# Kernel tuning notes

Hardware: AMD Instinct MI355X
Metric: run time of the kernel (lower is better)

## Reference

```python
import jax, jax.numpy as jnp
import numpy as np

BS, SEQ, IN, H = 16, 1024, 512, 512


def setup_inputs() -> dict:
    key = jax.random.key(0)
    ks = jax.random.split(key, 10)
    std = 1.0 / np.sqrt(H)
    u = lambda k, shape: jax.random.uniform(k, shape, jnp.float32, -std, std)
    return {
        "x": jax.random.normal(ks[0], (BS, SEQ, IN), jnp.float32),
        # input projection fc: input_size -> hidden_size
        "Wfc": u(ks[1], (IN, H)),
        "bfc": u(ks[2], (H,)),
        # cell 1 (main hidden stream h): tree of matmuls + gated elementwise
        "W1x": u(ks[3], (2 * H, H)),  # layer-0 cells see duplicated features (2H)
        "W1h": u(ks[4], (H, H)),
        "W1g": u(ks[5], (H, H)),
        # cell 2 (second hidden stream c)
        "W2x": u(ks[6], (2 * H, H)),
        "W2h": u(ks[7], (H, H)),
        "W2g": u(ks[8], (H, H)),
    }


def reference(x, Wfc, bfc, W1x, W1h, W1g, W2x, W2h, W2g):
    bs = x.shape[0]
    # layer-0 input prep: fc projection then feature duplication (cat([x,x],dim=2))
    xp = x @ Wfc + bfc                      # [bs, seq, H]
    xp = jnp.concatenate([xp, xp], axis=-1)  # [bs, seq, 2H]
    xs = jnp.swapaxes(xp, 0, 1)             # [seq, bs, 2H] for scan over time

    h0 = jnp.zeros((bs, H), x.dtype)
    c0 = jnp.zeros((bs, H), x.dtype)

    def step(carry, x_t):
        h, c = carry  # hidden streams x2, x3 fed to each evolved cell
        h_new = jnp.tanh(x_t @ W1x + h @ W1h + jax.nn.sigmoid(c @ W1g) * h)
        c_new = jax.nn.sigmoid(x_t @ W2x + c @ W2h) * jnp.tanh(h @ W2g)
        return (h_new, c_new), h_new  # hidden_seq collects stream 0

    (h_fin, c_fin), hseq = jax.lax.scan(step, (h0, c0), xs)
    out = jnp.swapaxes(hseq, 0, 1)  # batch_first: [bs, seq, H]
    # final hidden states: [num_layers*(1), bs, H] per main stream
    return out, h_fin[None], c_fin[None]
```

## Files before the change

kernel.cpp:

```cpp
#include <hip/hip_runtime.h>


typedef unsigned short u16;
typedef unsigned int   u32;
typedef __attribute__((ext_vector_type(8))) short s8v;
typedef __attribute__((ext_vector_type(4))) float f4v;

__device__ __forceinline__ u16 f2bf_rne(float f){
  u32 u = __float_as_uint(f);
  u32 r = u + 0x7fffu + ((u >> 16) & 1u);
  return (u16)(r >> 16);
}
__device__ __forceinline__ float bf2f(u16 h){ return __uint_as_float(((u32)h) << 16); }
__device__ __forceinline__ f4v MFMA(s8v a, s8v b, f4v c){
  return __builtin_amdgcn_mfma_f32_16x16x32_bf16(a, b, c, 0, 0, 0);
}
__device__ __forceinline__ float sigmoidf_(float x){ return 1.0f / (1.0f + __expf(-x)); }
__device__ __forceinline__ float tanh_fast(float x){
  float e = __expf(2.0f * x);
  return 1.0f - 2.0f / (e + 1.0f);
}

template<bool CC> __device__ __forceinline__ s8v ld16(const u16* p){
  s8v r;
  if (CC) asm volatile("global_load_dwordx4 %0, %1, off sc0 sc1" : "=v"(r) : "v"(p));
  else    asm volatile("global_load_dwordx4 %0, %1, off"         : "=v"(r) : "v"(p));
  return r;
}
template<bool CC> __device__ __forceinline__ void st2(u16* p, u32 v){
  if (CC) asm volatile("global_store_short %0, %1, off sc0 sc1" :: "v"(p), "v"(v) : "memory");
  else    asm volatile("global_store_short %0, %1, off"         :: "v"(p), "v"(v) : "memory");
}
__device__ __forceinline__ void store_dword_cc(u32* p, u32 v){
  asm volatile("global_store_dword %0, %1, off sc0 sc1" :: "v"(p), "v"(v) : "memory");
}
__device__ __forceinline__ void store_dword_plain_wait(u32* p, u32 v){
  asm volatile("global_store_dword %0, %1, off\n\ts_waitcnt vmcnt(0)"
               :: "v"(p), "v"(v) : "memory");
}
__device__ __forceinline__ u32 load_dword_plain_wait(const u32* p){
  u32 r;
  asm volatile("global_load_dword %0, %1, off\n\ts_waitcnt vmcnt(0)"
               : "=v"(r) : "v"(p));
  return r;
}

#define SEQT 1024
#define NWG  16
#define PROT 16

static const size_t OFF_U1  = 0;
static const size_t OFF_U2  = 33554432;
static const size_t OFF_WCT = OFF_U2 + 16777216;
static const size_t OFF_ST  = OFF_WCT;
static const size_t OFF_WT  = OFF_WCT + 1048576;
static const size_t OFF_BC  = OFF_WT + 2097152;
static const size_t OFF_FL  = OFF_BC + 4096;
static const size_t OFF_TOK = OFF_FL + 65536;
static const size_t OFF_PRS = OFF_TOK + 4096;
static const size_t OFF_CTL = OFF_PRS + 4096;
static const size_t OFF_CN  = OFF_CTL + 4096;
static const size_t OFF_HCN = OFF_CN + 4096;
static const size_t OFF_CCN = OFF_HCN + 131072;

__global__ void wcombk(const float* __restrict__ Wfc, const float* __restrict__ W1x,
                       const float* __restrict__ W2x, u16* __restrict__ Wct){
  __shared__ float A[16][17], B[16][17];
  const float* Wx = blockIdx.z ? W2x : W1x;
  int i0 = blockIdx.y * 16, n0 = blockIdx.x * 16;
  int tx = threadIdx.x, ty = threadIdx.y;
  float acc = 0.f;
  for (int kc = 0; kc < 512; kc += 16){
    A[ty][tx] = Wfc[(size_t)(i0 + ty) * 512 + kc + tx];
    B[ty][tx] = Wx[(size_t)(kc + ty) * 512 + n0 + tx]
              + Wx[(size_t)(kc + ty + 512) * 512 + n0 + tx];
    __syncthreads();
    #pragma unroll
    for (int kk = 0; kk < 16; ++kk) acc += A[ty][kk] * B[kk][tx];
    __syncthreads();
  }
  Wct[(size_t)(blockIdx.z * 512 + n0 + tx) * 512 + i0 + ty] = f2bf_rne(acc);
}

__global__ void bcombk(const float* __restrict__ bfc, const float* __restrict__ W1x,
                       const float* __restrict__ W2x, float* __restrict__ bc){
  int n = blockIdx.x * 256 + threadIdx.x;
  const float* Wx = (n < 512) ? W1x : W2x;
  int nl = n & 511;
  float acc = 0.f;
  for (int k = 0; k < 512; ++k)
    acc += bfc[k] * (Wx[(size_t)k * 512 + nl] + Wx[(size_t)(k + 512) * 512 + nl]);
  bc[n] = acc;
}

__global__ void wtk(const float* __restrict__ A, const float* __restrict__ B,
                    const float* __restrict__ C, const float* __restrict__ D,
                    u16* __restrict__ Wt){
  __shared__ float tile[32][33];
  const float* src = (blockIdx.z == 0) ? A : (blockIdx.z == 1) ? B
                    : (blockIdx.z == 2) ? C : D;
  int n0 = blockIdx.x * 32, k0 = blockIdx.y * 32;
  for (int i = threadIdx.y; i < 32; i += 8)
    tile[i][threadIdx.x] = src[(size_t)(k0 + i) * 512 + n0 + threadIdx.x];
  __syncthreads();
  for (int i = threadIdx.y; i < 32; i += 8)
    Wt[(size_t)blockIdx.z * 262144 + (size_t)(n0 + i) * 512 + k0 + threadIdx.x]
        = f2bf_rne(tile[threadIdx.x][i]);
}

__global__ __launch_bounds__(256) void gemmk(
    const float* __restrict__ x, const u16* __restrict__ Wct,
    const float* __restrict__ bc, float* __restrict__ U1, u16* __restrict__ U2){
  int l = threadIdx.x & 63, w = threadIdx.x >> 6;
  int lr = l & 15, lk = l >> 4;
  int m0 = blockIdx.y * 128 + (w & 1) * 64;
  int n0 = blockIdx.x * 64 + (w >> 1) * 32;
  f4v acc[4][2] = {};
  for (int ks = 0; ks < 16; ++ks){
    int k0 = ks * 32 + lk * 8;
    s8v bh0 = *(const s8v*)(Wct + (size_t)(n0 + lr) * 512 + k0);
    s8v bh1 = *(const s8v*)(Wct + (size_t)(n0 + 16 + lr) * 512 + k0);
    #pragma unroll
    for (int mi = 0; mi < 4; ++mi){
      const float* xp = x + (size_t)(m0 + mi * 16 + lr) * 512 + k0;
      f4v v0 = *(const f4v*)xp;
      f4v v1 = *(const f4v*)(xp + 4);
      s8v ah, al;
      #pragma unroll
      for (int j = 0; j < 4; ++j){
        { u32 u = __float_as_uint(v0[j]); ah[j] = (short)(u >> 16);
          float lof = v0[j] - __uint_as_float(u & 0xffff0000u);
          al[j] = (short)(__float_as_uint(lof) >> 16); }
        { u32 u = __float_as_uint(v1[j]); ah[j + 4] = (short)(u >> 16);
          float lof = v1[j] - __uint_as_float(u & 0xffff0000u);
          al[j + 4] = (short)(__float_as_uint(lof) >> 16); }
      }
      acc[mi][0] = MFMA(ah, bh0, acc[mi][0]);
      acc[mi][0] = MFMA(al, bh0, acc[mi][0]);
      acc[mi][1] = MFMA(ah, bh1, acc[mi][1]);
      acc[mi][1] = MFMA(al, bh1, acc[mi][1]);
    }
  }
  #pragma unroll
  for (int mi = 0; mi < 4; ++mi)
    #pragma unroll
    for (int ni = 0; ni < 2; ++ni){
      int n = n0 + ni * 16 + lr;
      float badd = bc[n];
      #pragma unroll
      for (int j = 0; j < 4; ++j){
        int r = m0 + mi * 16 + lk * 4 + j;
        int b = r >> 10, t = r & 1023;
        size_t oi = (size_t)(t * 16 + b) * 512;
        float v = acc[mi][ni][j] + badd;
        if (n < 512) U1[oi + n] = v;
        else         U2[oi + n - 512] = f2bf_rne(v);
      }
    }
}

__device__ __forceinline__ void poll_cnt(u32* p, u32 need, int l){
  int g = 0;
  for (;;){
    u32 v = 0;
    if (l == 0)
      v = __hip_atomic_fetch_add(p, 0x10000u, __ATOMIC_RELAXED,
                                 __HIP_MEMORY_SCOPE_WORKGROUP);
    v = __builtin_amdgcn_readfirstlane(v);
    if ((v & 0xffffu) >= need) break;
    if (++g > 4000000) break;
    __builtin_amdgcn_s_sleep(1);
  }
}
__device__ __forceinline__ void tok_store(u32* tok, u32 v){
  __hip_atomic_store(tok, v, __ATOMIC_RELEASE, __HIP_MEMORY_SCOPE_WORKGROUP);
}
__device__ __forceinline__ void spin_tok(u32* tok, u32 need){
  int g = 0;
  while (__hip_atomic_load(tok, __ATOMIC_ACQUIRE, __HIP_MEMORY_SCOPE_WORKGROUP) < need){
    if (++g > 16000000) break;
  }
}

__device__ __forceinline__ void heater(const u32* done){
  float a0 = 1.0f + (float)(threadIdx.x & 7) * 1e-7f;
  float a1 = 1.5f;
  float m = 0.9999999f, b = 1e-7f;
  for (int it = 0; it < 600000; ++it){
    #pragma unroll
    for (int k = 0; k < 32; ++k){
      asm volatile("v_fmac_f32 %0, %2, %3\n\tv_fmac_f32 %1, %2, %3"
                   : "+v"(a0), "+v"(a1) : "v"(m), "v"(b));
    }
    if ((it & 15) == 0){
      if (__hip_atomic_load(done, __ATOMIC_RELAXED, __HIP_MEMORY_SCOPE_AGENT) != 0u)
        break;
    }
  }
  asm volatile("" :: "v"(a0), "v"(a1));
}

__device__ __forceinline__ void scan_fast(
    int wg, int tid,
    const float* __restrict__ U1, const u16* __restrict__ U2,
    const u16* __restrict__ Wt, u16* __restrict__ st,
    u32* __restrict__ hcnt, u32* __restrict__ ccnt,
    float* __restrict__ out, float* xg, float* xt, u32* ltok){
  const int w = tid >> 6, l = tid & 63;
  const int lr = l & 15, lk = l >> 4;
  const int ncol0 = wg * 32 + lr;

  s8v bf0[16], bf1[16];
  {
    const u16* Wm = Wt + (size_t)w * (512 * 512);
    #pragma unroll
    for (int ks = 0; ks < 16; ++ks){
      bf0[ks] = *(const s8v*)(Wm + (size_t)ncol0 * 512 + ks * 32 + lk * 8);
      bf1[ks] = *(const s8v*)(Wm + (size_t)(ncol0 + 16) * 512 + ks * 32 + lk * 8);
    }
  }
  const bool useH = (w == 0) || (w == 3);
  float hp0[4] = {0, 0, 0, 0}, hp1[4] = {0, 0, 0, 0};

  float un0[4], un1[4], uc0[4], uc1[4];
  u32   ur0[4], ur1[4];
  if (w == 0){
    #pragma unroll
    for (int j = 0; j < 4; ++j){
      size_t ro = (size_t)(lk * 4 + j) * 512;
      un0[j] = U1[ro + ncol0];
      un1[j] = U1[ro + ncol0 + 16];
    }
  } else if (w == 2){
    #pragma unroll
    for (int j = 0; j < 4; ++j){
      size_t ro = (size_t)(lk * 4 + j) * 512;
      ur0[j] = U2[ro + ncol0];
      ur1[j] = U2[ro + ncol0 + 16];
    }
  }

  for (int t = 0; t < SEQT; ++t){
    if (w == 0){
      if (t > 0) poll_cnt(hcnt + (size_t)(t - 1) * 32, NWG, l);
      tok_store(ltok + 0, (u32)(t + 1));
    } else if (w == 2){
      if (t > 0) poll_cnt(ccnt + (size_t)(t - 1) * 32, NWG, l);
      tok_store(ltok + 1, (u32)(t + 1));
    } else if (w == 3){
      spin_tok(ltok + 0, (u32)(t + 1));
    } else {
      spin_tok(ltok + 1, (u32)(t + 1));
    }
    __builtin_amdgcn_sched_barrier(0);

    u16* rb = st + (size_t)(t & (PROT - 1)) * 32768 + (useH ? 0 : 16384);
    s8v ah[16], al[16];
    {
      u16* bhp = rb + lr * 512 + lk * 8;
      u16* blp = rb + 8192 + lr * 512 + lk * 8;
      #pragma unroll
      for (int ks = 0; ks < 16; ++ks){
        ah[ks] = ld16<false>(bhp + ks * 32);
        al[ks] = ld16<false>(blp + ks * 32);
      }
    }
    asm volatile("s_waitcnt vmcnt(0)" ::: "memory");
    __builtin_amdgcn_sched_barrier(0);

    if (w == 0){
      #pragma unroll
      for (int j = 0; j < 4; ++j){ uc0[j] = un0[j]; uc1[j] = un1[j]; }
    } else if (w == 2){
      #pragma unroll
      for (int j = 0; j < 4; ++j){
        uc0[j] = __uint_as_float(ur0[j] << 16);
        uc1[j] = __uint_as_float(ur1[j] << 16);
      }
    }

    f4v a0 = {0, 0, 0, 0}, a1 = {0, 0, 0, 0};
    f4v b0 = {0, 0, 0, 0}, b1 = {0, 0, 0, 0};
    #pragma unroll
    for (int ks = 0; ks < 16; ++ks){
      a0 = MFMA(ah[ks], bf0[ks], a0);
      a1 = MFMA(ah[ks], bf1[ks], a1);
      b0 = MFMA(al[ks], bf0[ks], b0);
      b1 = MFMA(al[ks], bf1[ks], b1);
    }
    #pragma unroll
    for (int j = 0; j < 4; ++j){ a0[j] += b0[j]; a1[j] += b1[j]; }

    const int par = t & 1;
    u16* wb = st + (size_t)((t + 1) & (PROT - 1)) * 32768;
    const int tn = (t + 1 < SEQT) ? t + 1 : t;

    if (w == 1){
      #pragma unroll
      for (int j = 0; j < 4; ++j){
        xg[((par * 2 + 0) * 16 + lk * 4 + j) * 16 + lr] = sigmoidf_(a0[j]);
        xg[((par * 2 + 1) * 16 + lk * 4 + j) * 16 + lr] = sigmoidf_(a1[j]);
      }
      tok_store(ltok + 2, (u32)(t + 1));
    } else if (w == 3){
      #pragma unroll
      for (int j = 0; j < 4; ++j){
        xt[((par * 2 + 0) * 16 + lk * 4 + j) * 16 + lr] = tanh_fast(a0[j]);
        xt[((par * 2 + 1) * 16 + lk * 4 + j) * 16 + lr] = tanh_fast(a1[j]);
      }
      tok_store(ltok + 3, (u32)(t + 1));
    } else if (w == 0){
      spin_tok(ltok + 2, (u32)(t + 1));
      __builtin_amdgcn_sched_barrier(0);
      float hn0v[4], hn1v[4];
      #pragma unroll
      for (int j = 0; j < 4; ++j){
        int b = lk * 4 + j;
        float hn0 = tanh_fast(uc0[j] + a0[j] + xg[((par * 2 + 0) * 16 + b) * 16 + lr] * hp0[j]);
        float hn1 = tanh_fast(uc1[j] + a1[j] + xg[((par * 2 + 1) * 16 + b) * 16 + lr] * hp1[j]);
        hp0[j] = hn0; hp1[j] = hn1;
        hn0v[j] = hn0; hn1v[j] = hn1;
        u32 u0 = __float_as_uint(hn0), u1 = __float_as_uint(hn1);
        int bi = b * 512;
        st2<false>(wb + bi + ncol0,      u0 >> 16);
        st2<false>(wb + bi + ncol0 + 16, u1 >> 16);
        float lo0 = hn0 - __uint_as_float(u0 & 0xffff0000u);
        float lo1 = hn1 - __uint_as_float(u1 & 0xffff0000u);
        st2<false>(wb + 8192 + bi + ncol0,      __float_as_uint(lo0) >> 16);
        st2<false>(wb + 8192 + bi + ncol0 + 16, __float_as_uint(lo1) >> 16);
      }
      #pragma unroll
      for (int j = 0; j < 4; ++j){
        size_t ro = (size_t)(tn * 16 + lk * 4 + j) * 512;
        un0[j] = U1[ro + ncol0];
        un1[j] = U1[ro + ncol0 + 16];
      }
      asm volatile("s_waitcnt vmcnt(8)" ::: "memory");
      if (l == 0)
        __hip_atomic_fetch_add(hcnt + (size_t)t * 32, 1u,
                               __ATOMIC_RELAXED, __HIP_MEMORY_SCOPE_WORKGROUP);
      #pragma unroll
      for (int j = 0; j < 4; ++j){
        int b = lk * 4 + j;
        size_t ob = (size_t)b * (SEQT * 512) + (size_t)t * 512;
        out[ob + ncol0]      = hn0v[j];
        out[ob + ncol0 + 16] = hn1v[j];
        if (t == SEQT - 1){
          out[8388608 + (size_t)b * 512 + ncol0]      = hn0v[j];
          out[8388608 + (size_t)b * 512 + ncol0 + 16] = hn1v[j];
        }
      }
    } else {
      spin_tok(ltok + 3, (u32)(t + 1));
      __builtin_amdgcn_sched_barrier(0);
      float cn0v[4], cn1v[4];
      #pragma unroll
      for (int j = 0; j < 4; ++j){
        int b = lk * 4 + j;
        float cn0 = sigmoidf_(uc0[j] + a0[j]) * xt[((par * 2 + 0) * 16 + b) * 16 + lr];
        float cn1 = sigmoidf_(uc1[j] + a1[j]) * xt[((par * 2 + 1) * 16 + b) * 16 + lr];
        cn0v[j] = cn0; cn1v[j] = cn1;
        u32 u0 = __float_as_uint(cn0), u1 = __float_as_uint(cn1);
        int bi = b * 512;
        st2<false>(wb + 16384 + bi + ncol0,      u0 >> 16);
        st2<false>(wb + 16384 + bi + ncol0 + 16, u1 >> 16);
        float lo0 = cn0 - __uint_as_float(u0 & 0xffff0000u);
        float lo1 = cn1 - __uint_as_float(u1 & 0xffff0000u);
        st2<false>(wb + 24576 + bi + ncol0,      __float_as_uint(lo0) >> 16);
        st2<false>(wb + 24576 + bi + ncol0 + 16, __float_as_uint(lo1) >> 16);
      }
      #pragma unroll
      for (int j = 0; j < 4; ++j){
        size_t ro = (size_t)(tn * 16 + lk * 4 + j) * 512;
        ur0[j] = U2[ro + ncol0];
        ur1[j] = U2[ro + ncol0 + 16];
      }
      asm volatile("s_waitcnt vmcnt(8)" ::: "memory");
      if (l == 0)
        __hip_atomic_fetch_add(ccnt + (size_t)t * 32, 1u,
                               __ATOMIC_RELAXED, __HIP_MEMORY_SCOPE_WORKGROUP);
      if (t == SEQT - 1){
        #pragma unroll
        for (int j = 0; j < 4; ++j){
          int b = lk * 4 + j;
          out[8396800 + (size_t)b * 512 + ncol0]      = cn0v[j];
          out[8396800 + (size_t)b * 512 + ncol0 + 16] = cn1v[j];
        }
      }
    }
  }
}

__device__ __forceinline__ void scan_cc(
    int wg, int tid,
    const float* __restrict__ U1, const u16* __restrict__ U2,
    const u16* __restrict__ Wt, u16* __restrict__ st,
    u32* __restrict__ flags, float* __restrict__ out, float* xg, float* xt){
  const int w = tid >> 6, l = tid & 63;
  const int lr = l & 15, lk = l >> 4;
  const int ncol0 = wg * 32 + lr;
  s8v bf0[16], bf1[16];
  {
    const u16* Wm = Wt + (size_t)w * (512 * 512);
    #pragma unroll
    for (int ks = 0; ks < 16; ++ks){
      bf0[ks] = *(const s8v*)(Wm + (size_t)ncol0 * 512 + ks * 32 + lk * 8);
      bf1[ks] = *(const s8v*)(Wm + (size_t)(ncol0 + 16) * 512 + ks * 32 + lk * 8);
    }
  }
  const bool useH = (w == 0) || (w == 3);
  float hp0[4] = {0, 0, 0, 0}, hp1[4] = {0, 0, 0, 0};
  long guard = 0;
  for (int t = 0; t < SEQT; ++t){
    float uu0[4], uu1[4];
    if (w == 0){
      #pragma unroll
      for (int j = 0; j < 4; ++j){
        size_t ro = (size_t)(t * 16 + lk * 4 + j) * 512;
        uu0[j] = U1[ro + ncol0];
        uu1[j] = U1[ro + ncol0 + 16];
      }
    } else if (w == 2){
      #pragma unroll
      for (int j = 0; j < 4; ++j){
        size_t ro = (size_t)(t * 16 + lk * 4 + j) * 512;
        uu0[j] = bf2f(U2[ro + ncol0]);
        uu1[j] = bf2f(U2[ro + ncol0 + 16]);
      }
    }
    if (t > 0){
      const u32* fl = flags + (size_t)(t - 1) * NWG;
      for (;;){
        u32 v = 1u;
        if (l < NWG) v = __hip_atomic_load(fl + l, __ATOMIC_RELAXED, __HIP_MEMORY_SCOPE_AGENT);
        if (__all(v != 0u)) break;
        if (++guard > 1000000L) break;
      }
      __builtin_amdgcn_sched_barrier(0);
    }
    u16* rb = st + (size_t)(t & (PROT - 1)) * 32768 + (useH ? 0 : 16384);
    s8v ah[16], al[16];
    {
      u16* bhp = rb + lr * 512 + lk * 8;
      u16* blp = rb + 8192 + lr * 512 + lk * 8;
      #pragma unroll
      for (int ks = 0; ks < 16; ++ks){
        ah[ks] = ld16<true>(bhp + ks * 32);
        al[ks] = ld16<true>(blp + ks * 32);
      }
    }
    asm volatile("s_waitcnt vmcnt(0)" ::: "memory");
    __builtin_amdgcn_sched_barrier(0);
    f4v a0 = {0, 0, 0, 0}, a1 = {0, 0, 0, 0};
    f4v b0 = {0, 0, 0, 0}, b1 = {0, 0, 0, 0};
    #pragma unroll
    for (int ks = 0; ks < 16; ++ks){
      a0 = MFMA(ah[ks], bf0[ks], a0);
      a1 = MFMA(ah[ks], bf1[ks], a1);
      b0 = MFMA(al[ks], bf0[ks], b0);
      b1 = MFMA(al[ks], bf1[ks], b1);
    }
    #pragma unroll
    for (int j = 0; j < 4; ++j){ a0[j] += b0[j]; a1[j] += b1[j]; }
    if (w == 1){
      #pragma unroll
      for (int j = 0; j < 4; ++j){
        xg[(0 * 16 + lk * 4 + j) * 16 + lr] = sigmoidf_(a0[j]);
        xg[(1 * 16 + lk * 4 + j) * 16 + lr] = sigmoidf_(a1[j]);
      }
    } else if (w == 3){
      #pragma unroll
      for (int j = 0; j < 4; ++j){
        xt[(0 * 16 + lk * 4 + j) * 16 + lr] = tanh_fast(a0[j]);
        xt[(1 * 16 + lk * 4 + j) * 16 + lr] = tanh_fast(a1[j]);
      }
    }
    __syncthreads();
    u16* wb = st + (size_t)((t + 1) & (PROT - 1)) * 32768;
    float hn0v[4], hn1v[4], cn0v[4], cn1v[4];
    if (w == 0){
      #pragma unroll
      for (int j = 0; j < 4; ++j){
        int b = lk * 4 + j;
        float hn0 = tanh_fast(uu0[j] + a0[j] + xg[(0 * 16 + b) * 16 + lr] * hp0[j]);
        float hn1 = tanh_fast(uu1[j] + a1[j] + xg[(1 * 16 + b) * 16 + lr] * hp1[j]);
        hp0[j] = hn0; hp1[j] = hn1;
        hn0v[j] = hn0; hn1v[j] = hn1;
        u32 u0 = __float_as_uint(hn0), u1 = __float_as_uint(hn1);
        int bi = b * 512;
        st2<true>(wb + bi + ncol0,      u0 >> 16);
        st2<true>(wb + bi + ncol0 + 16, u1 >> 16);
        float lo0 = hn0 - __uint_as_float(u0 & 0xffff0000u);
        float lo1 = hn1 - __uint_as_float(u1 & 0xffff0000u);
        st2<true>(wb + 8192 + bi + ncol0,      __float_as_uint(lo0) >> 16);
        st2<true>(wb + 8192 + bi + ncol0 + 16, __float_as_uint(lo1) >> 16);
      }
      asm volatile("s_waitcnt vmcnt(0)" ::: "memory");
    } else if (w == 2){
      #pragma unroll
      for (int j = 0; j < 4; ++j){
        int b = lk * 4 + j;
        float cn0 = sigmoidf_(uu0[j] + a0[j]) * xt[(0 * 16 + b) * 16 + lr];
        float cn1 = sigmoidf_(uu1[j] + a1[j]) * xt[(1 * 16 + b) * 16 + lr];
        cn0v[j] = cn0; cn1v[j] = cn1;
        u32 u0 = __float_as_uint(cn0), u1 = __float_as_uint(cn1);
        int bi = b * 512;
        st2<true>(wb + 16384 + bi + ncol0,      u0 >> 16);
        st2<true>(wb + 16384 + bi + ncol0 + 16, u1 >> 16);
        float lo0 = cn0 - __uint_as_float(u0 & 0xffff0000u);
        float lo1 = cn1 - __uint_as_float(u1 & 0xffff0000u);
        st2<true>(wb + 24576 + bi + ncol0,      __float_as_uint(lo0) >> 16);
        st2<true>(wb + 24576 + bi + ncol0 + 16, __float_as_uint(lo1) >> 16);
      }
      asm volatile("s_waitcnt vmcnt(0)" ::: "memory");
    }
    __syncthreads();
    if (tid == 0) store_dword_cc(flags + (size_t)t * NWG + wg, 1u);
    if (w == 0){
      #pragma unroll
      for (int j = 0; j < 4; ++j){
        int b = lk * 4 + j;
        size_t ob = (size_t)b * (SEQT * 512) + (size_t)t * 512;
        out[ob + ncol0]      = hn0v[j];
        out[ob + ncol0 + 16] = hn1v[j];
        if (t == SEQT - 1){
          out[8388608 + (size_t)b * 512 + ncol0]      = hn0v[j];
          out[8388608 + (size_t)b * 512 + ncol0 + 16] = hn1v[j];
        }
      }
    } else if (w == 2 && t == SEQT - 1){
      #pragma unroll
      for (int j = 0; j < 4; ++j){
        int b = lk * 4 + j;
        out[8396800 + (size_t)b * 512 + ncol0]      = cn0v[j];
        out[8396800 + (size_t)b * 512 + ncol0 + 16] = cn1v[j];
      }
    }
  }
}

__global__ __launch_bounds__(256, 1) void recurk(
    const float* __restrict__ U1, const u16* __restrict__ U2,
    const u16* __restrict__ Wt, u16* __restrict__ st,
    u32* __restrict__ flags, u32* __restrict__ hcnt, u32* __restrict__ ccnt,
    u32* __restrict__ tok, u32* __restrict__ prs,
    u32* __restrict__ ctl, float* __restrict__ out){
  const int tid = threadIdx.x;
  __shared__ int slot_sh, mode_sh;
  __shared__ float xg[4 * 16 * 16], xt[4 * 16 * 16];
  __shared__ u32 ltok[4];
  u32* cntp  = ctl;
  u32* modep = ctl + 16;
  u32* donep = ctl + 64;

  if (tid == 0){
    int s = -1;
    u32 xcc;
    asm volatile("s_getreg_b32 %0, hwreg(HW_REG_XCC_ID)" : "=s"(xcc));
    if ((xcc & 0xfu) == 0u)
      s = (int)__hip_atomic_fetch_add(cntp, 1u, __ATOMIC_RELAXED,
                                      __HIP_MEMORY_SCOPE_AGENT);
    slot_sh = s;
  }
  __syncthreads();
  const int slot = slot_sh;

  if (tid == 0){
    if (slot >= 0 && slot < NWG){
      store_dword_plain_wait(tok + slot * 16, 0x5A5A0000u + (u32)slot);
      __hip_atomic_store(prs + slot * 16, 1u, __ATOMIC_RELAXED,
                         __HIP_MEMORY_SCOPE_AGENT);
    }
    if (blockIdx.x == 0){
      long g = 0;
      for (;;){
        u32 c = __hip_atomic_load(cntp, __ATOMIC_RELAXED, __HIP_MEMORY_SCOPE_AGENT);
        if (c >= NWG) break;
        if (++g > 2000000L){ atomicCAS(modep, 0u, 2u); break; }
      }
    }
    if (slot == 0){
      bool ok = true;
      long g = 0;
      for (int s2 = 1; s2 < NWG && ok; ++s2){
        for (;;){
          u32 p = __hip_atomic_load(prs + s2 * 16, __ATOMIC_RELAXED,
                                    __HIP_MEMORY_SCOPE_AGENT);
          if (p) break;
          if (++g > 5000000L){ ok = false; break; }
        }
      }
      if (ok){
        for (int s2 = 1; s2 < NWG; ++s2){
          u32 v = load_dword_plain_wait(tok + s2 * 16);
          if (v != 0x5A5A0000u + (u32)s2){ ok = false; break; }
        }
      }
      atomicCAS(modep, 0u, ok ? 1u : 3u);
    }
    long g = 0;
    u32 m;
    for (;;){
      m = __hip_atomic_load(modep, __ATOMIC_RELAXED, __HIP_MEMORY_SCOPE_AGENT);
      if (m) break;
      if (++g > 50000000L){ m = 3u; break; }
    }
    mode_sh = (int)m;
  }
  if (tid < 4) ltok[tid] = 0;
  __syncthreads();
  const int mode = mode_sh;

  int wg; bool part;
  if (mode == 2){ wg = blockIdx.x; part = (wg < NWG); }
  else          { wg = slot;       part = (slot >= 0 && slot < NWG); }

  if (!part){
    heater(donep);
    return;
  }

  if (mode == 1) scan_fast(wg, tid, U1, U2, Wt, st, hcnt, ccnt, out, xg, xt, ltok);
  else           scan_cc (wg, tid, U1, U2, Wt, st, flags, out, xg, xt);

  if (wg == 0 && tid == 0)
    __hip_atomic_store(donep, 1u, __ATOMIC_RELAXED, __HIP_MEMORY_SCOPE_AGENT);
}

extern "C" void kernel_launch(void* const* d_in, const int* in_sizes, int n_in,
                              void* d_out, int out_size, void* d_ws, size_t ws_size,
                              hipStream_t stream){
  const float* x   = (const float*)d_in[0];
  const float* Wfc = (const float*)d_in[1];
  const float* bfc = (const float*)d_in[2];
  const float* W1x = (const float*)d_in[3];
  const float* W1h = (const float*)d_in[4];
  const float* W1g = (const float*)d_in[5];
  const float* W2x = (const float*)d_in[6];
  const float* W2h = (const float*)d_in[7];
  const float* W2g = (const float*)d_in[8];

  char* ws = (char*)d_ws;
  float* U1   = (float*)(ws + OFF_U1);
  u16*   U2   = (u16*)  (ws + OFF_U2);
  u16*   Wct  = (u16*)  (ws + OFF_WCT);
  u16*   st   = (u16*)  (ws + OFF_ST);
  u16*   Wt   = (u16*)  (ws + OFF_WT);
  float* bc   = (float*)(ws + OFF_BC);
  u32*   flags= (u32*)  (ws + OFF_FL);
  u32*   tok  = (u32*)  (ws + OFF_TOK);
  u32*   prs  = (u32*)  (ws + OFF_PRS);
  u32*   ctl  = (u32*)  (ws + OFF_CTL);
  u32*   hcnt = (u32*)  (ws + OFF_HCN);
  u32*   ccnt = (u32*)  (ws + OFF_CCN);
  float* out  = (float*)d_out;

  hipMemsetAsync(ws + OFF_FL, 0, 65536 + 4096 + 4096 + 4096 + 4096, stream);
  hipMemsetAsync(ws + OFF_HCN, 0, 262144, stream);

  wcombk<<<dim3(32, 32, 2), dim3(16, 16), 0, stream>>>(Wfc, W1x, W2x, Wct);
  bcombk<<<dim3(4), dim3(256), 0, stream>>>(bfc, W1x, W2x, bc);
  wtk   <<<dim3(16, 16, 4), dim3(32, 8), 0, stream>>>(W1h, W1g, W2h, W2g, Wt);
  gemmk <<<dim3(16, 128), dim3(256), 0, stream>>>(x, Wct, bc, U1, U2);
  hipMemsetAsync(ws + OFF_ST, 0, 1048576, stream);
  recurk<<<dim3(256), dim3(256), 0, stream>>>(U1, U2, Wt, st, flags, hcnt, ccnt, tok, prs, ctl, out);
}
```

Before: 6.230 ms.

## Split recurrent step into four batch groups pipelined with per-group counters

The persistent recurrent kernel's fast path now processes the 16 batch rows as four groups of four, each with its own cross-workgroup arrival counter and local token slots. A group can start its matmul as soon as that group's slice of the previous step has been published, so sync latency overlaps with compute on other groups. A probe via fetch-add reads ahead whether the counter is already complete so the poll can be skipped. The cost is four times as many MFMA passes over partially replicated A rows, more atomics, and larger counter and shared buffers.

```diff
diff --git a/kernel.cpp b/kernel.cpp
--- a/kernel.cpp
+++ b/kernel.cpp
@@ -48,6 +48,7 @@
 #define SEQT 1024
 #define NWG  16
 #define PROT 16
+#define NG   4
 
 static const size_t OFF_U1  = 0;
 static const size_t OFF_U2  = 33554432;
@@ -61,7 +62,7 @@
 static const size_t OFF_CTL = OFF_PRS + 4096;
 static const size_t OFF_CN  = OFF_CTL + 4096;
 static const size_t OFF_HCN = OFF_CN + 4096;
-static const size_t OFF_CCN = OFF_HCN + 131072;
+static const size_t OFF_CCN = OFF_HCN + 262144;
 
 __global__ void wcombk(const float* __restrict__ Wfc, const float* __restrict__ W1x,
                        const float* __restrict__ W2x, u16* __restrict__ Wct){
@@ -209,6 +210,7 @@
   const int w = tid >> 6, l = tid & 63;
   const int lr = l & 15, lk = l >> 4;
   const int ncol0 = wg * 32 + lr;
+  const int arow = (lr & 3);
 
   s8v bf0[16], bf1[16];
   {
@@ -219,173 +221,275 @@
       bf1[ks] = *(const s8v*)(Wm + (size_t)(ncol0 + 16) * 512 + ks * 32 + lk * 8);
     }
   }
-  const bool useH = (w == 0) || (w == 3);
-  float hp0[4] = {0, 0, 0, 0}, hp1[4] = {0, 0, 0, 0};
-
-  float un0[4], un1[4], uc0[4], uc1[4];
-  u32   ur0[4], ur1[4];
+
   if (w == 0){
-    #pragma unroll
-    for (int j = 0; j < 4; ++j){
-      size_t ro = (size_t)(lk * 4 + j) * 512;
-      un0[j] = U1[ro + ncol0];
-      un1[j] = U1[ro + ncol0 + 16];
+    float hp0[NG][4] = {}, hp1[NG][4] = {};
+    float un0[NG][4], un1[NG][4];
+    u32 probe[NG] = {NWG, NWG, NWG, NWG};
+    #pragma unroll
+    for (int g = 0; g < NG; ++g)
+      #pragma unroll
+      for (int j = 0; j < 4; ++j){
+        size_t ro = (size_t)(g * 4 + j) * 512;
+        un0[g][j] = U1[ro + ncol0];
+        un1[g][j] = U1[ro + ncol0 + 16];
+      }
+    for (int t = 0; t < SEQT; ++t){
+      const int par = t & 1, slot = t & (PROT - 1), wslot = (t + 1) & (PROT - 1);
+      const int tn = (t + 1 < SEQT) ? t + 1 : t;
+      #pragma unroll
+      for (int g = 0; g < NG; ++g){
+        const int ai = t * NG + g;
+        if (t > 0 && (probe[g] & 0xffffu) < NWG)
+          poll_cnt(hcnt + (size_t)(ai - NG) * 16, NWG, l);
+        if (ai >= NG - 1){
+          u32 v = 0;
+          if (l == 0)
+            v = __hip_atomic_fetch_add(hcnt + (size_t)(ai - (NG - 1)) * 16, 0x10000u,
+                                       __ATOMIC_RELAXED, __HIP_MEMORY_SCOPE_WORKGROUP);
+          probe[(g + 1) & (NG - 1)] = __builtin_amdgcn_readfirstlane(v);
+        }
+        tok_store(ltok + g * 4 + 0, (u32)(t + 1));
+        s8v ah[16], al[16];
+        {
+          const u16* bhp = st + (size_t)slot * 32768
+                         + (size_t)(g * 4 + arow) * 512 + lk * 8;
+          #pragma unroll
+          for (int ks = 0; ks < 16; ++ks){
+            ah[ks] = ld16<false>(bhp + ks * 32);
+            al[ks] = ld16<false>(bhp + 8192 + ks * 32);
+          }
+        }
+        asm volatile("s_waitcnt vmcnt(0)" ::: "memory");
+        __builtin_amdgcn_sched_barrier(0);
+        float uc0[4], uc1[4];
+        #pragma unroll
+        for (int j = 0; j < 4; ++j){ uc0[j] = un0[g][j]; uc1[j] = un1[g][j]; }
+        f4v a0 = {0,0,0,0}, a1 = {0,0,0,0}, b0 = {0,0,0,0}, b1 = {0,0,0,0};
+        #pragma unroll
+        for (int ks = 0; ks < 16; ++ks){
+          a0 = MFMA(ah[ks], bf0[ks], a0);
+          a1 = MFMA(ah[ks], bf1[ks], a1);
+          b0 = MFMA(al[ks], bf0[ks], b0);
+          b1 = MFMA(al[ks], bf1[ks], b1);
+        }
+        #pragma unroll
+        for (int j = 0; j < 4; ++j){ a0[j] += b0[j]; a1[j] += b1[j]; }
+        spin_tok(ltok + g * 4 + 2, (u32)(t + 1));
+        __builtin_amdgcn_sched_barrier(0);
+        u16* wb = st + (size_t)wslot * 32768;
+        float hn0v[4], hn1v[4];
+        #pragma unroll
+        for (int j = 0; j < 4; ++j){
+          float g0 = xg[((g * 2 + par) * 2 + 0) * 64 + j * 16 + lr];
+          float g1 = xg[((g * 2 + par) * 2 + 1) * 64 + j * 16 + lr];
+          float hn0 = tanh_fast(uc0[j] + a0[j] + g0 * hp0[g][j]);
+          float hn1 = tanh_fast(uc1[j] + a1[j] + g1 * hp1[g][j]);
+          hp0[g][j] = hn0; hp1[g][j] = hn1;
+          hn0v[j] = hn0; hn1v[j] = hn1;
+          if (lk == 0){
+            u32 u0 = __float_as_uint(hn0), u1 = __float_as_uint(hn1);
+            int bi = (g * 4 + j) * 512;
+            st2<false>(wb + bi + ncol0,      u0 >> 16);
+            st2<false>(wb + bi + ncol0 + 16, u1 >> 16);
+            float lo0 = hn0 - __uint_as_float(u0 & 0xffff0000u);
+            float lo1 = hn1 - __uint_as_float(u1 & 0xffff0000u);
+            st2<false>(wb + 8192 + bi + ncol0,      __float_as_uint(lo0) >> 16);
+            st2<false>(wb + 8192 + bi + ncol0 + 16, __float_as_uint(lo1) >> 16);
+          }
+        }
+        #pragma unroll
+        for (int j = 0; j < 4; ++j){
+          size_t ro = (size_t)(tn * 16 + g * 4 + j) * 512;
+          un0[g][j] = U1[ro + ncol0];
+          un1[g][j] = U1[ro + ncol0 + 16];
+        }
+        asm volatile("s_waitcnt vmcnt(8)" ::: "memory");
+        if (l == 0)
+          __hip_atomic_fetch_add(hcnt + (size_t)ai * 16, 1u,
+                                 __ATOMIC_RELAXED, __HIP_MEMORY_SCOPE_WORKGROUP);
+        if (lk == 0){
+          #pragma unroll
+          for (int j = 0; j < 4; ++j){
+            size_t ob = (size_t)(g * 4 + j) * (SEQT * 512) + (size_t)t * 512;
+            out[ob + ncol0]      = hn0v[j];
+            out[ob + ncol0 + 16] = hn1v[j];
+            if (t == SEQT - 1){
+              out[8388608 + (size_t)(g * 4 + j) * 512 + ncol0]      = hn0v[j];
+              out[8388608 + (size_t)(g * 4 + j) * 512 + ncol0 + 16] = hn1v[j];
+            }
+          }
+        }
+      }
     }
   } else if (w == 2){
-    #pragma unroll
-    for (int j = 0; j < 4; ++j){
-      size_t ro = (size_t)(lk * 4 + j) * 512;
-      ur0[j] = U2[ro + ncol0];
-      ur1[j] = U2[ro + ncol0 + 16];
-    }
-  }
-
-  for (int t = 0; t < SEQT; ++t){
-    if (w == 0){
-      if (t > 0) poll_cnt(hcnt + (size_t)(t - 1) * 32, NWG, l);
-      tok_store(ltok + 0, (u32)(t + 1));
-    } else if (w == 2){
-      if (t > 0) poll_cnt(ccnt + (size_t)(t - 1) * 32, NWG, l);
-      tok_store(ltok + 1, (u32)(t + 1));
-    } else if (w == 3){
-      spin_tok(ltok + 0, (u32)(t + 1));
-    } else {
-      spin_tok(ltok + 1, (u32)(t + 1));
-    }
-    __builtin_amdgcn_sched_barrier(0);
-
-    u16* rb = st + (size_t)(t & (PROT - 1)) * 32768 + (useH ? 0 : 16384);
-    s8v ah[16], al[16];
-    {
-      u16* bhp = rb + lr * 512 + lk * 8;
-      u16* blp = rb + 8192 + lr * 512 + lk * 8;
-      #pragma unroll
-      for (int ks = 0; ks < 16; ++ks){
-        ah[ks] = ld16<false>(bhp + ks * 32);
-        al[ks] = ld16<false>(blp + ks * 32);
-      }
-    }
-    asm volatile("s_waitcnt vmcnt(0)" ::: "memory");
-    __builtin_amdgcn_sched_barrier(0);
-
-    if (w == 0){
-      #pragma unroll
-      for (int j = 0; j < 4; ++j){ uc0[j] = un0[j]; uc1[j] = un1[j]; }
-    } else if (w == 2){
-      #pragma unroll
-      for (int j = 0; j < 4; ++j){
-        uc0[j] = __uint_as_float(ur0[j] << 16);
-        uc1[j] = __uint_as_float(ur1[j] << 16);
-      }
-    }
-
-    f4v a0 = {0, 0, 0, 0}, a1 = {0, 0, 0, 0};
-    f4v b0 = {0, 0, 0, 0}, b1 = {0, 0, 0, 0};
-    #pragma unroll
-    for (int ks = 0; ks < 16; ++ks){
-      a0 = MFMA(ah[ks], bf0[ks], a0);
-      a1 = MFMA(ah[ks], bf1[ks], a1);
-      b0 = MFMA(al[ks], bf0[ks], b0);
-      b1 = MFMA(al[ks], bf1[ks], b1);
-    }
-    #pragma unroll
-    for (int j = 0; j < 4; ++j){ a0[j] += b0[j]; a1[j] += b1[j]; }
-
-    const int par = t & 1;
-    u16* wb = st + (size_t)((t + 1) & (PROT - 1)) * 32768;
-    const int tn = (t + 1 < SEQT) ? t + 1 : t;
-
-    if (w == 1){
-      #pragma unroll
-      for (int j = 0; j < 4; ++j){
-        xg[((par * 2 + 0) * 16 + lk * 4 + j) * 16 + lr] = sigmoidf_(a0[j]);
-        xg[((par * 2 + 1) * 16 + lk * 4 + j) * 16 + lr] = sigmoidf_(a1[j]);
-      }
-      tok_store(ltok + 2, (u32)(t + 1));
-    } else if (w == 3){
-      #pragma unroll
-      for (int j = 0; j < 4; ++j){
-        xt[((par * 2 + 0) * 16 + lk * 4 + j) * 16 + lr] = tanh_fast(a0[j]);
-        xt[((par * 2 + 1) * 16 + lk * 4 + j) * 16 + lr] = tanh_fast(a1[j]);
-      }
-      tok_store(ltok + 3, (u32)(t + 1));
-    } else if (w == 0){
-      spin_tok(ltok + 2, (u32)(t + 1));
-      __builtin_amdgcn_sched_barrier(0);
-      float hn0v[4], hn1v[4];
-      #pragma unroll
-      for (int j = 0; j < 4; ++j){
-        int b = lk * 4 + j;
-        float hn0 = tanh_fast(uc0[j] + a0[j] + xg[((par * 2 + 0) * 16 + b) * 16 + lr] * hp0[j]);
-        float hn1 = tanh_fast(uc1[j] + a1[j] + xg[((par * 2 + 1) * 16 + b) * 16 + lr] * hp1[j]);
-        hp0[j] = hn0; hp1[j] = hn1;
-        hn0v[j] = hn0; hn1v[j] = hn1;
-        u32 u0 = __float_as_uint(hn0), u1 = __float_as_uint(hn1);
-        int bi = b * 512;
-        st2<false>(wb + bi + ncol0,      u0 >> 16);
-        st2<false>(wb + bi + ncol0 + 16, u1 >> 16);
-        float lo0 = hn0 - __uint_as_float(u0 & 0xffff0000u);
-        float lo1 = hn1 - __uint_as_float(u1 & 0xffff0000u);
-        st2<false>(wb + 8192 + bi + ncol0,      __float_as_uint(lo0) >> 16);
-        st2<false>(wb + 8192 + bi + ncol0 + 16, __float_as_uint(lo1) >> 16);
-      }
-      #pragma unroll
-      for (int j = 0; j < 4; ++j){
-        size_t ro = (size_t)(tn * 16 + lk * 4 + j) * 512;
-        un0[j] = U1[ro + ncol0];
-        un1[j] = U1[ro + ncol0 + 16];
-      }
-      asm volatile("s_waitcnt vmcnt(8)" ::: "memory");
-      if (l == 0)
-        __hip_atomic_fetch_add(hcnt + (size_t)t * 32, 1u,
-                               __ATOMIC_RELAXED, __HIP_MEMORY_SCOPE_WORKGROUP);
-      #pragma unroll
-      for (int j = 0; j < 4; ++j){
-        int b = lk * 4 + j;
-        size_t ob = (size_t)b * (SEQT * 512) + (size_t)t * 512;
-        out[ob + ncol0]      = hn0v[j];
-        out[ob + ncol0 + 16] = hn1v[j];
-        if (t == SEQT - 1){
-          out[8388608 + (size_t)b * 512 + ncol0]      = hn0v[j];
-          out[8388608 + (size_t)b * 512 + ncol0 + 16] = hn1v[j];
-        }
-      }
-    } else {
-      spin_tok(ltok + 3, (u32)(t + 1));
-      __builtin_amdgcn_sched_barrier(0);
-      float cn0v[4], cn1v[4];
-      #pragma unroll
-      for (int j = 0; j < 4; ++j){
-        int b = lk * 4 + j;
-        float cn0 = sigmoidf_(uc0[j] + a0[j]) * xt[((par * 2 + 0) * 16 + b) * 16 + lr];
-        float cn1 = sigmoidf_(uc1[j] + a1[j]) * xt[((par * 2 + 1) * 16 + b) * 16 + lr];
-        cn0v[j] = cn0; cn1v[j] = cn1;
-        u32 u0 = __float_as_uint(cn0), u1 = __float_as_uint(cn1);
-        int bi = b * 512;
-        st2<false>(wb + 16384 + bi + ncol0,      u0 >> 16);
-        st2<false>(wb + 16384 + bi + ncol0 + 16, u1 >> 16);
-        float lo0 = cn0 - __uint_as_float(u0 & 0xffff0000u);
-        float lo1 = cn1 - __uint_as_float(u1 & 0xffff0000u);
-        st2<false>(wb + 24576 + bi + ncol0,      __float_as_uint(lo0) >> 16);
-        st2<false>(wb + 24576 + bi + ncol0 + 16, __float_as_uint(lo1) >> 16);
-      }
-      #pragma unroll
-      for (int j = 0; j < 4; ++j){
-        size_t ro = (size_t)(tn * 16 + lk * 4 + j) * 512;
-        ur0[j] = U2[ro + ncol0];
-        ur1[j] = U2[ro + ncol0 + 16];
-      }
-      asm volatile("s_waitcnt vmcnt(8)" ::: "memory");
-      if (l == 0)
-        __hip_atomic_fetch_add(ccnt + (size_t)t * 32, 1u,
-                               __ATOMIC_RELAXED, __HIP_MEMORY_SCOPE_WORKGROUP);
-      if (t == SEQT - 1){
+    u32 ur0[NG][4], ur1[NG][4];
+    u32 probe[NG] = {NWG, NWG, NWG, NWG};
+    #pragma unroll
+    for (int g = 0; g < NG; ++g)
+      #pragma unroll
+      for (int j = 0; j < 4; ++j){
+        size_t ro = (size_t)(g * 4 + j) * 512;
+        ur0[g][j] = U2[ro + ncol0];
+        ur1[g][j] = U2[ro + ncol0 + 16];
+      }
+    for (int t = 0; t < SEQT; ++t){
+      const int par = t & 1, slot = t & (PROT - 1), wslot = (t + 1) & (PROT - 1);
+      const int tn = (t + 1 < SEQT) ? t + 1 : t;
+      #pragma unroll
+      for (int g = 0; g < NG; ++g){
+        const int ai = t * NG + g;
+        if (t > 0 && (probe[g] & 0xffffu) < NWG)
+          poll_cnt(ccnt + (size_t)(ai - NG) * 16, NWG, l);
+        if (ai >= NG - 1){
+          u32 v = 0;
+          if (l == 0)
+            v = __hip_atomic_fetch_add(ccnt + (size_t)(ai - (NG - 1)) * 16, 0x10000u,
+                                       __ATOMIC_RELAXED, __HIP_MEMORY_SCOPE_WORKGROUP);
+          probe[(g + 1) & (NG - 1)] = __builtin_amdgcn_readfirstlane(v);
+        }
+        tok_store(ltok + g * 4 + 1, (u32)(t + 1));
+        s8v ah[16], al[16];
+        {
+          const u16* bhp = st + (size_t)slot * 32768 + 16384
+                         + (size_t)(g * 4 + arow) * 512 + lk * 8;
+          #pragma unroll
+          for (int ks = 0; ks < 16; ++ks){
+            ah[ks] = ld16<false>(bhp + ks * 32);
+            al[ks] = ld16<false>(bhp + 8192 + ks * 32);
+          }
+        }
+        asm volatile("s_waitcnt vmcnt(0)" ::: "memory");
+        __builtin_amdgcn_sched_barrier(0);
+        float uc0[4], uc1[4];
         #pragma unroll
         for (int j = 0; j < 4; ++j){
-          int b = lk * 4 + j;
-          out[8396800 + (size_t)b * 512 + ncol0]      = cn0v[j];
-          out[8396800 + (size_t)b * 512 + ncol0 + 16] = cn1v[j];
-        }
+          uc0[j] = __uint_as_float(ur0[g][j] << 16);
+          uc1[j] = __uint_as_float(ur1[g][j] << 16);
+        }
+        f4v a0 = {0,0,0,0}, a1 = {0,0,0,0}, b0 = {0,0,0,0}, b1 = {0,0,0,0};
+        #pragma unroll
+        for (int ks = 0; ks < 16; ++ks){
+          a0 = MFMA(ah[ks], bf0[ks], a0);
+          a1 = MFMA(ah[ks], bf1[ks], a1);
+          b0 = MFMA(al[ks], bf0[ks], b0);
+          b1 = MFMA(al[ks], bf1[ks], b1);
+        }
+        #pragma unroll
+        for (int j = 0; j < 4; ++j){ a0[j] += b0[j]; a1[j] += b1[j]; }
+        spin_tok(ltok + g * 4 + 3, (u32)(t + 1));
+        __builtin_amdgcn_sched_barrier(0);
+        u16* wb = st + (size_t)wslot * 32768;
+        float cn0v[4], cn1v[4];
+        #pragma unroll
+        for (int j = 0; j < 4; ++j){
+          float x0 = xt[((g * 2 + par) * 2 + 0) * 64 + j * 16 + lr];
+          float x1 = xt[((g * 2 + par) * 2 + 1) * 64 + j * 16 + lr];
+          float cn0 = sigmoidf_(uc0[j] + a0[j]) * x0;
+          float cn1 = sigmoidf_(uc1[j] + a1[j]) * x1;
+          cn0v[j] = cn0; cn1v[j] = cn1;
+          if (lk == 0){
+            u32 u0 = __float_as_uint(cn0), u1 = __float_as_uint(cn1);
+            int bi = (g * 4 + j) * 512;
+            st2<false>(wb + 16384 + bi + ncol0,      u0 >> 16);
+            st2<false>(wb + 16384 + bi + ncol0 + 16, u1 >> 16);
+            float lo0 = cn0 - __uint_as_float(u0 & 0xffff0000u);
+            float lo1 = cn1 - __uint_as_float(u1 & 0xffff0000u);
+            st2<false>(wb + 24576 + bi + ncol0,      __float_as_uint(lo0) >> 16);
+            st2<false>(wb + 24576 + bi + ncol0 + 16, __float_as_uint(lo1) >> 16);
+          }
+        }
+        #pragma unroll
+        for (int j = 0; j < 4; ++j){
+          size_t ro = (size_t)(tn * 16 + g * 4 + j) * 512;
+          ur0[g][j] = U2[ro + ncol0];
+          ur1[g][j] = U2[ro + ncol0 + 16];
+        }
+        asm volatile("s_waitcnt vmcnt(8)" ::: "memory");
+        if (l == 0)
+          __hip_atomic_fetch_add(ccnt + (size_t)ai * 16, 1u,
+                                 __ATOMIC_RELAXED, __HIP_MEMORY_SCOPE_WORKGROUP);
+        if (lk == 0 && t == SEQT - 1){
+          #pragma unroll
+          for (int j = 0; j < 4; ++j){
+            out[8396800 + (size_t)(g * 4 + j) * 512 + ncol0]      = cn0v[j];
+            out[8396800 + (size_t)(g * 4 + j) * 512 + ncol0 + 16] = cn1v[j];
+          }
+        }
+      }
+    }
+  } else if (w == 1){
+    for (int t = 0; t < SEQT; ++t){
+      const int par = t & 1, slot = t & (PROT - 1);
+      #pragma unroll
+      for (int g = 0; g < NG; ++g){
+        spin_tok(ltok + g * 4 + 1, (u32)(t + 1));
+        __builtin_amdgcn_sched_barrier(0);
+        s8v ah[16], al[16];
+        {
+          const u16* bhp = st + (size_t)slot * 32768 + 16384
+                         + (size_t)(g * 4 + arow) * 512 + lk * 8;
+          #pragma unroll
+          for (int ks = 0; ks < 16; ++ks){
+            ah[ks] = ld16<false>(bhp + ks * 32);
+            al[ks] = ld16<false>(bhp + 8192 + ks * 32);
+          }
+        }
+        asm volatile("s_waitcnt vmcnt(0)" ::: "memory");
+        __builtin_amdgcn_sched_barrier(0);
+        f4v a0 = {0,0,0,0}, a1 = {0,0,0,0}, b0 = {0,0,0,0}, b1 = {0,0,0,0};
+        #pragma unroll
+        for (int ks = 0; ks < 16; ++ks){
+          a0 = MFMA(ah[ks], bf0[ks], a0);
+          a1 = MFMA(ah[ks], bf1[ks], a1);
+          b0 = MFMA(al[ks], bf0[ks], b0);
+          b1 = MFMA(al[ks], bf1[ks], b1);
+        }
+        if (lk == 0){
+          #pragma unroll
+          for (int j = 0; j < 4; ++j){
+            xg[((g * 2 + par) * 2 + 0) * 64 + j * 16 + lr] = sigmoidf_(a0[j] + b0[j]);
+            xg[((g * 2 + par) * 2 + 1) * 64 + j * 16 + lr] = sigmoidf_(a1[j] + b1[j]);
+          }
+        }
+        tok_store(ltok + g * 4 + 2, (u32)(t + 1));
+      }
+    }
+  } else {
+    for (int t = 0; t < SEQT; ++t){
+      const int par = t & 1, slot = t & (PROT - 1);
+      #pragma unroll
+      for (int g = 0; g < NG; ++g){
+        spin_tok(ltok + g * 4 + 0, (u32)(t + 1));
+        __builtin_amdgcn_sched_barrier(0);
+        s8v ah[16], al[16];
+        {
+          const u16* bhp = st + (size_t)slot * 32768
+                         + (size_t)(g * 4 + arow) * 512 + lk * 8;
+          #pragma unroll
+          for (int ks = 0; ks < 16; ++ks){
+            ah[ks] = ld16<false>(bhp + ks * 32);
+            al[ks] = ld16<false>(bhp + 8192 + ks * 32);
+          }
+        }
+        asm volatile("s_waitcnt vmcnt(0)" ::: "memory");
+        __builtin_amdgcn_sched_barrier(0);
+        f4v a0 = {0,0,0,0}, a1 = {0,0,0,0}, b0 = {0,0,0,0}, b1 = {0,0,0,0};
+        #pragma unroll
+        for (int ks = 0; ks < 16; ++ks){
+          a0 = MFMA(ah[ks], bf0[ks], a0);
+          a1 = MFMA(ah[ks], bf1[ks], a1);
+          b0 = MFMA(al[ks], bf0[ks], b0);
+          b1 = MFMA(al[ks], bf1[ks], b1);
+        }
+        if (lk == 0){
+          #pragma unroll
+          for (int j = 0; j < 4; ++j){
+            xt[((g * 2 + par) * 2 + 0) * 64 + j * 16 + lr] = tanh_fast(a0[j] + b0[j]);
+            xt[((g * 2 + par) * 2 + 1) * 64 + j * 16 + lr] = tanh_fast(a1[j] + b1[j]);
+          }
+        }
+        tok_store(ltok + g * 4 + 3, (u32)(t + 1));
       }
     }
   }
@@ -451,8 +555,7 @@
     }
     asm volatile("s_waitcnt vmcnt(0)" ::: "memory");
     __builtin_amdgcn_sched_barrier(0);
-    f4v a0 = {0, 0, 0, 0}, a1 = {0, 0, 0, 0};
-    f4v b0 = {0, 0, 0, 0}, b1 = {0, 0, 0, 0};
+    f4v a0 = {0,0,0,0}, a1 = {0,0,0,0}, b0 = {0,0,0,0}, b1 = {0,0,0,0};
     #pragma unroll
     for (int ks = 0; ks < 16; ++ks){
       a0 = MFMA(ah[ks], bf0[ks], a0);
@@ -547,8 +650,8 @@
     u32* __restrict__ ctl, float* __restrict__ out){
   const int tid = threadIdx.x;
   __shared__ int slot_sh, mode_sh;
-  __shared__ float xg[4 * 16 * 16], xt[4 * 16 * 16];
-  __shared__ u32 ltok[4];
+  __shared__ float xg[1024], xt[1024];
+  __shared__ u32 ltok[16];
   u32* cntp  = ctl;
   u32* modep = ctl + 16;
   u32* donep = ctl + 64;
@@ -607,7 +710,7 @@
     }
     mode_sh = (int)m;
   }
-  if (tid < 4) ltok[tid] = 0;
+  if (tid < 16) ltok[tid] = 0;
   __syncthreads();
   const int mode = mode_sh;
 
@@ -656,7 +759,7 @@
   float* out  = (float*)d_out;
 
   hipMemsetAsync(ws + OFF_FL, 0, 65536 + 4096 + 4096 + 4096 + 4096, stream);
-  hipMemsetAsync(ws + OFF_HCN, 0, 262144, stream);
+  hipMemsetAsync(ws + OFF_HCN, 0, 524288, stream);
 
   wcombk<<<dim3(32, 32, 2), dim3(16, 16), 0, stream>>>(Wfc, W1x, W2x, Wct);
   bcombk<<<dim3(4), dim3(256), 0, stream>>>(bfc, W1x, W2x, bc);
```

Result: slower. 21.40 ms (+243.5%).
